# Performance work log

Measured on AMD Instinct MI355X. Metric: run time of the kernel, lower is better.

The kernel has to match this reference:

```python
import jax, jax.numpy as jnp
import numpy as np
import math

MUL = 16                      # num_in_features == num_out_features
LDIMS = (1, 3, 5)             # 0e, 1o, 2e  (lmax = 2)
FEAT = MUL * sum(LDIMS)       # 144 = irreps dim = number_of_basis
PATHS = [(0,0,0),(1,1,0),(2,2,0),
         (0,1,1),(1,0,1),(1,2,1),(2,1,1),
         (0,2,2),(1,1,2),(2,0,2),(2,2,2)]
DOT_PATHS = [(0,0,0),(1,1,0),(2,2,0)]

# ---------- real Wigner-3j / Clebsch-Gordan (e3nn convention), numpy precompute ----------

def _su2_cg(j1, m1, j2, m2, j3, m3):
    if m3 != m1 + m2:
        return 0.0
    f = math.factorial
    vmin = max(-j1 + j2 + m3, -j1 + m1, 0)
    vmax = min(j2 + j3 + m1, j3 - j1 + j2, j3 + m3)
    C = math.sqrt((2*j3+1) * f(j3+j1-j2) * f(j3-j1+j2) * f(j1+j2-j3)
                  * f(j3+m3) * f(j3-m3)
                  / (f(j1+j2+j3+1) * f(j1-m1) * f(j1+m1) * f(j2-m2) * f(j2+m2)))
    S = 0.0
    for v in range(vmin, vmax + 1):
        S += (-1.0)**(v + j2 + m2) * f(j2+j3+m1-v) * f(j1-m1+v) / (
            f(v) * f(j3-j1+j2-v) * f(j3+m3-v) * f(v+j1-j2-m3))
    return C * S

def _qmat(l):
    # complex -> real spherical-harmonic change of basis (e3nn convention)
    q = np.zeros((2*l+1, 2*l+1), dtype=np.complex128)
    for m in range(-l, 0):
        q[l+m, l+abs(m)] = 1.0/math.sqrt(2)
        q[l+m, l-abs(m)] = -1j/math.sqrt(2)
    q[l, l] = 1.0
    for m in range(1, l+1):
        q[l+m, l+abs(m)] = (-1)**m/math.sqrt(2)
        q[l+m, l-abs(m)] = 1j*(-1)**m/math.sqrt(2)
    return (-1j)**l * q

def _real_w3j(l1, l2, l3):
    C = np.zeros((2*l1+1, 2*l2+1, 2*l3+1))
    for i, m1 in enumerate(range(-l1, l1+1)):
        for j, m2 in enumerate(range(-l2, l2+1)):
            for k, m3 in enumerate(range(-l3, l3+1)):
                C[i, j, k] = _su2_cg(l1, m1, l2, m2, l3, m3)
    Cr = np.einsum('ij,kl,mn,ikn->jlm', _qmat(l1), _qmat(l2),
                   np.conj(_qmat(l3).T), C.astype(np.complex128))
    Cr = np.real(Cr)
    return (Cr / np.linalg.norm(Cr)).astype(np.float32)  # unit Frobenius norm (3j convention)

W3J = {p: _real_w3j(*p) for p in set(PATHS)}

# ---------- fully connected tensor product (component/element normalization) ----------

def _split(x):
    # blocked layout: [mul x 0e | mul x 1o | mul x 2e]
    n = x.shape[0]
    xs, o = [], 0
    for d in LDIMS:
        xs.append(x[:, o:o + MUL*d].reshape(n, MUL, d))
        o += MUL * d
    return xs

def _fctp(x1, x2, W):
    # W: [11, u, v, w] stacked per PATHS
    xs1, xs2 = _split(x1), _split(x2)
    n = x1.shape[0]
    n_paths = {l3: sum(1 for p in PATHS if p[2] == l3) for l3 in range(3)}
    outs = [None, None, None]
    for i, (l1, l2, l3) in enumerate(PATHS):
        C = jnp.asarray(W3J[(l1, l2, l3)])          # [i, j, k]
        scale = math.sqrt((2*l3 + 1) / (n_paths[l3] * MUL * MUL))
        a = jnp.einsum('nvj,ijk->nivk', xs2[l2], C)      # [n, i, v, k]
        b = jnp.einsum('nui,nivk->nuvk', xs1[l1], a)     # [n, u, v, k]
        o = scale * jnp.einsum('nuvk,uvw->nwk', b, W[i]) # [n, w, k]
        outs[l3] = o if outs[l3] is None else outs[l3] + o
    return jnp.concatenate([o.reshape(n, -1) for o in outs], axis=1)  # [n, 9*MUL]

def _dot(x1, x2, Wd):
    # FCTP(irreps_input, irreps_input, '0e'): paths (0,0,0),(1,1,0),(2,2,0), out mul = 1
    xs1, xs2 = _split(x1), _split(x2)
    fan = 3 * MUL * MUL
    acc = 0.0
    for i, (l1, l2, l3) in enumerate(DOT_PATHS):
        C = jnp.asarray(W3J[(l1, l2, l3)])[:, :, 0]      # [i, j]
        t = jnp.einsum('nui,ij,nvj->nuv', xs1[l1], C, xs2[l2])
        acc = acc + jnp.einsum('nuv,uv->n', t, Wd[i])
    return (acc * math.sqrt(1.0 / fan))[:, None]         # [n, 1]

def setup_inputs() -> dict:
    key = jax.random.key(0)
    ks = jax.random.split(key, 8)
    N = 50000
    return {
        'nodes_features': jax.random.normal(ks[0], (N, FEAT), jnp.float32),
        'degree_matrix': jax.random.normal(ks[1], (N,), jnp.float32),
        'edges_features_distance': jax.random.normal(ks[2], (N,), jnp.float32),
        'edges_features_bond': jax.random.normal(ks[3], (N,), jnp.float32),
        'w_q': jax.random.normal(ks[4], (11, MUL, MUL, MUL), jnp.float32),
        'w_k': jax.random.normal(ks[5], (11, MUL, MUL, MUL), jnp.float32),
        'w_v': jax.random.normal(ks[6], (11, MUL, MUL, MUL), jnp.float32),
        'w_dot': jax.random.normal(ks[7], (3, MUL, MUL), jnp.float32),
    }

def reference(nodes_features, degree_matrix, edges_features_distance,
              edges_features_bond, w_q, w_k, w_v, w_dot):
    # degree_matrix / edges_features_* are unused by the original forward
    x = nodes_features
    q = _fctp(x, x, w_q)                   # tp_q(x, x)
    k = _fctp(x, x, w_k)                   # tp_k(x, x)
    v = _fctp(x, x, w_v)                   # tp(x, x)
    d = _dot(q, k, w_dot)                  # [n, 1]
    e = jnp.exp(d / math.sqrt(float(FEAT)))
    attn = e / (e + 1e-10)                 # sum over last dim of size 1 + eps
    out = attn * v                         # dropout is identity in eval mode
    out = out.reshape(-1, MUL)             # view(-1, num_heads * num_out_features)
    return jax.nn.elu(out)                 # [9n, MUL]
```

## Files before the change

kernel.cpp:

```cpp
#include <hip/hip_runtime.h>
#include <math.h>

#define NP 11
#define NN 8

__device__ __constant__ int g_l1[NP]   = {0,1,2,0,1,1,2,0,1,2,2};
__device__ __constant__ int g_l2[NP]   = {0,1,2,1,0,2,1,2,1,0,2};
__device__ __constant__ int g_l3[NP]   = {0,0,0,1,1,1,1,2,2,2,2};
__device__ __constant__ int g_coff[NP] = {0,1,10,35,44,53,98,143,168,213,238};

typedef _Float16 half8 __attribute__((ext_vector_type(8)));
typedef _Float16 h2 __attribute__((ext_vector_type(2)));
typedef float f32x4 __attribute__((ext_vector_type(4)));

__device__ __forceinline__ float bfu(unsigned int v){ return __uint_as_float(v<<16); }
__device__ __forceinline__ unsigned int rne16(float f){
  unsigned int ui=__float_as_uint(f);
  return (ui+0x7fffu+((ui>>16)&1u))>>16;
}
__device__ __forceinline__ unsigned short h16(float f){
  _Float16 h=(_Float16)f;
  return __builtin_bit_cast(unsigned short,h);
}
__device__ __forceinline__ float hf(unsigned short s){
  return (float)__builtin_bit_cast(_Float16,s);
}

__device__ double dfact(int n){ double r=1.0; for(int i=2;i<=n;++i) r*=(double)i; return r; }

__device__ double su2_cg(int j1,int m1,int j2,int m2,int j3,int m3){
  if(m1+m2!=m3) return 0.0;
  int vmin=-j1+j2+m3; if(-j1+m1>vmin) vmin=-j1+m1; if(vmin<0) vmin=0;
  int vmax=j2+j3+m1; int t=j3-j1+j2; if(t<vmax) vmax=t; t=j3+m3; if(t<vmax) vmax=t;
  double C = sqrt((double)(2*j3+1)*dfact(j3+j1-j2)*dfact(j3-j1+j2)*dfact(j1+j2-j3)
      *dfact(j3+m3)*dfact(j3-m3)
      /(dfact(j1+j2+j3+1)*dfact(j1-m1)*dfact(j1+m1)*dfact(j2-m2)*dfact(j2+m2)));
  double S=0.0;
  for(int v=vmin;v<=vmax;++v){
    double sg = ((v+j2+m2)&1)? -1.0:1.0;
    S += sg*dfact(j2+j3+m1-v)*dfact(j1-m1+v)
        /(dfact(v)*dfact(j3-j1+j2-v)*dfact(j3+m3-v)*dfact(v+j1-j2-m3));
  }
  return C*S;
}

__device__ void qelem(int l,int r,int c,double &re,double &im){
  int m=r-l; double a=0.0,b=0.0; const double s=0.70710678118654752440;
  if(m<0){ if(c==l-m) a=s; else if(c==l+m) b=-s; }
  else if(m==0){ if(c==l) a=1.0; }
  else { double sg=(m&1)?-1.0:1.0; if(c==l+m) a=sg*s; else if(c==l-m) b=sg*s; }
  if(l==1){ double tt=a; a=b; b=-tt; }
  else if(l==2){ a=-a; b=-b; }
  re=a; im=b;
}

__device__ int probe_f32(const unsigned short* __restrict__ p, int nelem, int* scnt){
  if(threadIdx.x==0) *scnt=0;
  __syncthreads();
  int M = nelem < 4096 ? nelem : 4096;
  int c=0;
  for(int t=threadIdx.x;t<M;t+=blockDim.x){
    unsigned e=((unsigned)p[t]>>7)&0xFFu;
    if(e!=0u && (e<0x70u || e>0x8Eu)) ++c;
  }
  atomicAdd(scnt,c);
  __syncthreads();
  return (*scnt*8 > M) ? 1 : 0;
}

__global__ void prep(const unsigned short* __restrict__ x,
                     const unsigned short* __restrict__ wq,
                     const unsigned short* __restrict__ wk,
                     const unsigned short* __restrict__ wv,
                     const unsigned short* __restrict__ wd,
                     int nx,int nw,int nd,
                     float* __restrict__ c3j, unsigned int* __restrict__ cgh,
                     unsigned int* __restrict__ wpre){
  const int p=blockIdx.x, tp=blockIdx.y;
  __shared__ double cg[125];
  __shared__ double outv[125];
  __shared__ double nrm;
  __shared__ int scnt;

  const unsigned short* ww=(tp==0)?wq:((tp==1)?wk:wv);
  const int f32 = probe_f32(ww,nw,&scnt);

  {
    unsigned int* dst=wpre+(size_t)(p*3+tp)*2240;
    for(int t=threadIdx.x;t<2048;t+=256){
      int w=t>>7, c=t&127;
      int i0=c*32+w, i1=i0+16;
      float f0,f1;
      if(f32){
        const float* wf=(const float*)ww+(size_t)p*4096;
        f0=wf[i0]; f1=wf[i1];
      }else{
        const unsigned short* wsp=ww+(size_t)p*4096;
        f0=bfu(wsp[i0]); f1=bfu(wsp[i1]);
      }
      dst[w*140+c]=(unsigned int)h16(f0)|((unsigned int)h16(f1)<<16);
    }
  }

  if(tp==0){
    int l1=g_l1[p], l2=g_l2[p], l3=g_l3[p];
    int d1=2*l1+1, d2=2*l2+1, d3=2*l3+1;
    int tot=d1*d2*d3;
    for(int t=threadIdx.x;t<tot;t+=256){
      int i=t/(d2*d3), k=(t/d3)%d2, n=t%d3;
      cg[t]=su2_cg(l1,i-l1,l2,k-l2,l3,n-l3);
    }
    __syncthreads();
    for(int t=threadIdx.x;t<tot;t+=256){
      int a=t/(d2*d3), b=(t/d3)%d2, c=t%d3;
      double sre=0.0;
      for(int i=0;i<d1;++i){ double q1r,q1i; qelem(l1,i,a,q1r,q1i);
        for(int k=0;k<d2;++k){ double q2r,q2i; qelem(l2,k,b,q2r,q2i);
          double pr=q1r*q2r-q1i*q2i, pi=q1r*q2i+q1i*q2r;
          for(int n=0;n<d3;++n){ double q3r,q3i; qelem(l3,n,c,q3r,q3i);
            sre += (pr*q3r + pi*q3i) * cg[(i*d2+k)*d3+n];
          }
        }
      }
      outv[t]=sre;
    }
    __syncthreads();
    if(threadIdx.x==0){
      double s=0.0; for(int t=0;t<tot;++t) s+=outv[t]*outv[t];
      nrm=sqrt(s);
    }
    __syncthreads();
    const float scl_[3]={0.03608439182435161f,0.05412658773652741f,0.06987712429686843f};
    float s=scl_[l3];
    for(int t=threadIdx.x;t<tot;t+=256){
      float val=(float)(outv[t]/nrm);
      c3j[g_coff[p]+t]=val;
      unsigned int h=(unsigned int)h16(val*s);
      cgh[g_coff[p]+t]=h|(h<<16);
    }
  }

  if(p==0 && tp==0){
    int xf=probe_f32(x,nx,&scnt);
    if(threadIdx.x==0) c3j[363]=(float)xf;
    int df=probe_f32(wd,nd,&scnt);
    if(threadIdx.x==0) c3j[367]=(float)df;
  }
}

#define L_AU   0
#define L_SO   5600
#define L_XP   7392
#define L_XD   8000
#define L_WD   9184
#define L_CG   9568
#define L_TOT  9932

template<int D1,int D2,int D3>
__device__ __forceinline__ void fusedAB(const unsigned int* __restrict__ lds,
                                        const unsigned int* __restrict__ cgp,
                                        unsigned int* __restrict__ sAu,
                                        int wave, int lane, int nvalid){
  constexpr int O1=(D1==1)?0:((D1==3)?16:64);
  constexpr int O2P=(D2==1)?0:((D2==3)?8:32);
  const int nn=lane>>3, vp=lane&7;
  if(nn>=nvalid) return;
  h2 x2p[D2];
  #pragma unroll
  for(int j=0;j<D2;++j) x2p[j]=__builtin_bit_cast(h2,lds[L_XP+nn*76+O2P+vp*D2+j]);
  const int u0=wave*2;
  h2 x1a[D1],x1b[D1];
  #pragma unroll
  for(int i=0;i<D1;++i){
    x1a[i]=__builtin_bit_cast(h2,lds[L_XD+nn*148+O1+u0*D1+i]);
    x1b[i]=__builtin_bit_cast(h2,lds[L_XD+nn*148+O1+(u0+1)*D1+i]);
  }
  h2 acc0[D3],acc1[D3];
  #pragma unroll
  for(int k=0;k<D3;++k){ acc0[k]=(h2){(_Float16)0.f,(_Float16)0.f}; acc1[k]=acc0[k]; }
  #pragma unroll
  for(int i=0;i<D1;++i){
    #pragma unroll
    for(int k=0;k<D3;++k){
      h2 ar=(h2){(_Float16)0.f,(_Float16)0.f};
      #pragma unroll
      for(int j=0;j<D2;++j)
        ar+=__builtin_bit_cast(h2,cgp[(i*D2+j)*D3+k])*x2p[j];
      acc0[k]+=x1a[i]*ar;
      acc1[k]+=x1b[i]*ar;
    }
  }
  #pragma unroll
  for(int k=0;k<D3;++k){
    sAu[(k*8+nn)*140+u0*8+vp]   =__builtin_bit_cast(unsigned int,acc0[k]);
    sAu[(k*8+nn)*140+u0*8+vp+8] =__builtin_bit_cast(unsigned int,acc1[k]);
  }
}

template<int L3>
__device__ __forceinline__ void stage2_acc(const unsigned int* __restrict__ sAu,
                                           const unsigned int* __restrict__ wp_path,
                                           f32x4& a0, f32x4& a1,
                                           int n16, int quad, int wave){
  constexpr int P=(L3+1)*3;
  if(wave<P){
    int tp=wave%3, Mt=wave/3;
    const unsigned int* ap=sAu+(Mt*16+n16)*140+quad*4;
    const uint4* bp=(const uint4*)(wp_path+tp*2240+n16*140+quad*4);
    uint4 b[8];
    #pragma unroll
    for(int ks=0;ks<8;++ks) b[ks]=bp[ks*4];
    f32x4 a=a0;
    #pragma unroll
    for(int ks=0;ks<8;++ks)
      a=__builtin_amdgcn_mfma_f32_16x16x32_f16(
          *reinterpret_cast<const half8*>(ap+ks*16),
          __builtin_bit_cast(half8,b[ks]),a,0,0,0);
    a0=a;
  }
  if(L3==2 && wave==0){
    const unsigned int* ap=sAu+(2*16+n16)*140+quad*4;
    const uint4* bp=(const uint4*)(wp_path+2*2240+n16*140+quad*4);
    uint4 b2[8];
    #pragma unroll
    for(int ks=0;ks<8;++ks) b2[ks]=bp[ks*4];
    f32x4 a=a1;
    #pragma unroll
    for(int ks=0;ks<8;++ks)
      a=__builtin_amdgcn_mfma_f32_16x16x32_f16(
          *reinterpret_cast<const half8*>(ap+ks*16),
          __builtin_bit_cast(half8,b2[ks]),a,0,0,0);
    a1=a;
  }
}

template<int L3>
__device__ __forceinline__ void stage2_out(const f32x4& a0, const f32x4& a1,
                                           unsigned short* __restrict__ sOh,
                                           int n16, int quad, int wave){
  constexpr int D3=2*L3+1;
  constexpr int OO=(L3==0)?0:((L3==1)?16:64);
  constexpr int P=(L3+1)*3;
  if(wave<P){
    int tp=wave%3, Mt=wave/3;
    #pragma unroll
    for(int reg=0;reg<4;++reg){
      int row=Mt*16+quad*4+reg;
      int k=row>>3, node=row&7;
      if(k<D3) sOh[node*448+tp*144+OO+n16*D3+k]=h16(a0[reg]);
    }
  }
  if(L3==2 && wave==0){
    #pragma unroll
    for(int reg=0;reg<4;++reg){
      int row=32+quad*4+reg;
      int k=row>>3, node=row&7;
      if(k<D3) sOh[node*448+2*144+OO+n16*D3+k]=h16(a1[reg]);
    }
  }
}

__global__ __launch_bounds__(512,8) void tfn_main(
    const unsigned short* __restrict__ xin,
    const unsigned int* __restrict__ wpre,
    const unsigned int* __restrict__ cgh,
    const unsigned short* __restrict__ wd,
    const float* __restrict__ c3j,
    unsigned short* __restrict__ outp, int N)
{
  __shared__ __align__(16) unsigned int lds[L_TOT];

  const int tid=threadIdx.x;
  const int wave=tid>>6, lane=tid&63;
  const int n16=lane&15, quad=lane>>4;
  const int node0=blockIdx.x*NN;
  const int nvalid=(N-node0)<NN?(N-node0):NN;

  const int xf32 = c3j[363]!=0.0f;
  const int df32 = c3j[367]!=0.0f;

  unsigned int* sAu=lds+L_AU;
  unsigned short* sOh=(unsigned short*)(lds+L_SO);
  unsigned short* sWdh=(unsigned short*)(lds+L_WD);

  float* scratch=(float*)(lds+L_SO);
  if(!xf32){
    for(int t=tid;t<NN*36;t+=512){
      int nn=t/36, w4=t%36;
      if(nn<nvalid){
        uint2 u=((const uint2*)(xin+(size_t)(node0+nn)*144))[w4];
        float* dst=&scratch[nn*144+w4*4];
        dst[0]=bfu(u.x&0xffffu); dst[1]=bfu(u.x>>16);
        dst[2]=bfu(u.y&0xffffu); dst[3]=bfu(u.y>>16);
      }
    }
  }else{
    const float* xf=(const float*)xin;
    for(int t=tid;t<NN*144;t+=512){
      int nn=t/144, f=t%144;
      if(nn<nvalid) scratch[nn*144+f]=xf[(size_t)(node0+nn)*144+f];
    }
  }
  if(!df32){ for(int t=tid;t<768;t+=512) sWdh[t]=(unsigned short)h16(bfu((unsigned int)wd[t])); }
  else     { const float* wdf=(const float*)wd; for(int t=tid;t<768;t+=512) sWdh[t]=(unsigned short)h16(wdf[t]); }
  for(int t=tid;t<363;t+=512) lds[L_CG+t]=cgh[t];
  __syncthreads();

  for(int t=tid;t<NN*144;t+=512){
    int nn=t/144, f=t-nn*144;
    unsigned int h=(unsigned int)h16(scratch[t]);
    lds[L_XD+nn*148+f]=h|(h<<16);
  }
  for(int t=tid;t<NN*72;t+=512){
    int nn=t/72, g=t-nn*72;
    int fa,fb;
    if(g<8){ fa=2*g; fb=fa+1; }
    else if(g<32){ int gg=g-8; int vp=gg/3, j=gg-3*vp; fa=16+(2*vp)*3+j; fb=fa+3; }
    else { int gg=g-32; int vp=gg/5, j=gg-5*vp; fa=64+(2*vp)*5+j; fb=fa+5; }
    lds[L_XP+nn*76+g]=(unsigned int)h16(scratch[nn*144+fa])|((unsigned int)h16(scratch[nn*144+fb])<<16);
  }
  __syncthreads();

  #define PATH_STEP(P_,D1_,D2_,D3_) { \
    fusedAB<D1_,D2_,D3_>(lds,lds+L_CG+g_coff[P_],sAu,wave,lane,nvalid); \
    __syncthreads(); \
    stage2_acc<(D3_-1)/2>(sAu,wpre+(size_t)P_*6720,a0,a1,n16,quad,wave); \
    __syncthreads(); }

  {
    f32x4 a0={0.f,0.f,0.f,0.f}, a1={0.f,0.f,0.f,0.f};
    PATH_STEP(0,1,1,1)
    PATH_STEP(1,3,3,1)
    PATH_STEP(2,5,5,1)
    stage2_out<0>(a0,a1,sOh,n16,quad,wave);
  }
  {
    f32x4 a0={0.f,0.f,0.f,0.f}, a1={0.f,0.f,0.f,0.f};
    PATH_STEP(3,1,3,3)
    PATH_STEP(4,3,1,3)
    PATH_STEP(5,3,5,3)
    PATH_STEP(6,5,3,3)
    stage2_out<1>(a0,a1,sOh,n16,quad,wave);
  }
  {
    f32x4 a0={0.f,0.f,0.f,0.f}, a1={0.f,0.f,0.f,0.f};
    PATH_STEP(7,1,5,5)
    PATH_STEP(8,3,3,5)
    PATH_STEP(9,5,1,5)
    PATH_STEP(10,5,5,5)
    stage2_out<2>(a0,a1,sOh,n16,quad,wave);
  }
  #undef PATH_STEP
  __syncthreads();

  {
    int node=wave;
    if(node<nvalid){
      const float c0=c3j[0], c1=c3j[1], c2=c3j[10];
      const unsigned short* qh=sOh+node*448;
      const unsigned short* kh=qh+144;
      const int v=lane&15, ug=lane>>4;
      float k0=hf(kh[v]);
      float k1[3],k2[5];
      #pragma unroll
      for(int j=0;j<3;++j) k1[j]=hf(kh[16+v*3+j]);
      #pragma unroll
      for(int m=0;m<5;++m) k2[m]=hf(kh[64+v*5+m]);
      float part=0.f;
      #pragma unroll
      for(int t=0;t<4;++t){
        int u=ug+4*t;
        float d0=hf(qh[u])*k0;
        float d1=0.f;
        #pragma unroll
        for(int j=0;j<3;++j) d1+=hf(qh[16+u*3+j])*k1[j];
        float d2=0.f;
        #pragma unroll
        for(int m=0;m<5;++m) d2+=hf(qh[64+u*5+m])*k2[m];
        part+=hf(sWdh[u*16+v])*(c0*d0)+hf(sWdh[256+u*16+v])*(c1*d1)+hf(sWdh[512+u*16+v])*(c2*d2);
      }
      #pragma unroll
      for(int off=1;off<64;off<<=1) part+=__shfl_xor(part,off,64);
      float dd=part*0.03608439182435161f;
      float ex=dd*(1.0f/12.0f);
      ex=fminf(fmaxf(ex,-80.f),80.f);
      float e=expf(ex);
      float attn=e/(e+1e-10f);
      const unsigned short* vh=qh+288;
      if(!xf32){
        unsigned short* ob=outp+(size_t)(node0+node)*144;
        for(int f=lane;f<144;f+=64){
          float val=attn*hf(vh[f]);
          float r=(val>0.f)?val:expm1f(val);
          ob[f]=(unsigned short)rne16(r);
        }
      }else{
        float* ob=(float*)outp+(size_t)(node0+node)*144;
        for(int f=lane;f<144;f+=64){
          float val=attn*hf(vh[f]);
          ob[f]=(val>0.f)?val:expm1f(val);
        }
      }
    }
  }
}

extern "C" void kernel_launch(void* const* d_in, const int* in_sizes, int n_in,
                              void* d_out, int out_size, void* d_ws, size_t ws_size,
                              hipStream_t stream){
  (void)n_in; (void)out_size; (void)ws_size;
  const unsigned short* x =(const unsigned short*)d_in[0];
  const unsigned short* wq=(const unsigned short*)d_in[4];
  const unsigned short* wk=(const unsigned short*)d_in[5];
  const unsigned short* wv=(const unsigned short*)d_in[6];
  const unsigned short* wd=(const unsigned short*)d_in[7];
  float* c3j=(float*)d_ws;
  unsigned int* cgh=(unsigned int*)d_ws+1024;
  unsigned int* wpre=(unsigned int*)d_ws+2048;
  int N=in_sizes[0]/144;
  prep<<<dim3(NP,3),dim3(256),0,stream>>>(x,wq,wk,wv,wd,
      in_sizes[0],in_sizes[4],in_sizes[7],c3j,cgh,wpre);
  int nb=(N+NN-1)/NN;
  tfn_main<<<dim3(nb),dim3(512),0,stream>>>(x,wpre,cgh,wd,c3j,(unsigned short*)d_out,N);
}
```

Measured before the change: 396.0 us.

## Fuse CG contraction into MFMA A-operand generation, removing per-path LDS staging and barriers

Each wave now computes its CG-contracted A fragment directly in registers and feeds it straight into MFMAs for all three weight sets, one (L3, M-tile) supertask per wave. This removes the shared-memory intermediate buffer and the two block barriers per path (22 in total). The CG table is re-laid out as [k][i][j] and padded. In exchange only 6 of 8 waves do work in this phase, per-wave register pressure rises, and launch bounds drop to 6 blocks per SM. Shared memory use shrinks.

After: 482.7 us. +21.9%, slower.

```diff
diff --git a/kernel.cpp b/kernel.cpp
--- a/kernel.cpp
+++ b/kernel.cpp
@@ -133,10 +133,11 @@
     const float scl_[3]={0.03608439182435161f,0.05412658773652741f,0.06987712429686843f};
     float s=scl_[l3];
     for(int t=threadIdx.x;t<tot;t+=256){
+      int a=t/(d2*d3), b=(t/d3)%d2, c=t%d3;
       float val=(float)(outv[t]/nrm);
       c3j[g_coff[p]+t]=val;
       unsigned int h=(unsigned int)h16(val*s);
-      cgh[g_coff[p]+t]=h|(h<<16);
+      cgh[g_coff[p]+c*(d1*d2)+a*d2+b]=h|(h<<16);
     }
   }
 
@@ -148,119 +149,107 @@
   }
 }
 
-#define L_AU   0
-#define L_SO   5600
-#define L_XP   7392
-#define L_XD   8000
-#define L_WD   9184
-#define L_CG   9568
-#define L_TOT  9932
-
-template<int D1,int D2,int D3>
-__device__ __forceinline__ void fusedAB(const unsigned int* __restrict__ lds,
-                                        const unsigned int* __restrict__ cgp,
-                                        unsigned int* __restrict__ sAu,
-                                        int wave, int lane, int nvalid){
+#define L_XP   0
+#define L_XD   608
+#define L_WD   1792
+#define L_CG   2176
+#define L_SO   2592
+#define L_SCR  4384
+#define L_TOT  8992
+
+template<int D1,int D2>
+__device__ __forceinline__ void path_mm(const unsigned int* __restrict__ lds,
+                                        int cgoff,
+                                        const unsigned int* __restrict__ wp_path,
+                                        f32x4* __restrict__ acc,
+                                        int n16,int quad,int Mt){
   constexpr int O1=(D1==1)?0:((D1==3)?16:64);
   constexpr int O2P=(D2==1)?0:((D2==3)?8:32);
-  const int nn=lane>>3, vp=lane&7;
-  if(nn>=nvalid) return;
-  h2 x2p[D2];
+  const int nn=n16&7;
+  const int k=Mt*2+(n16>>3);
+  h2 cg[D1*D2];
+  {
+    const unsigned int* cp=lds+L_CG+cgoff+k*(D1*D2);
+    #pragma unroll
+    for(int t=0;t<D1*D2;++t) cg[t]=__builtin_bit_cast(h2,cp[t]);
+  }
+  h2 x2[4*D2];
+  {
+    const unsigned int* xp=lds+L_XP+nn*76+O2P+(quad&1)*(4*D2);
+    #pragma unroll
+    for(int t=0;t<4*D2;++t) x2[t]=__builtin_bit_cast(h2,xp[t]);
+  }
+  h2 ar[4*D1];
   #pragma unroll
-  for(int j=0;j<D2;++j) x2p[j]=__builtin_bit_cast(h2,lds[L_XP+nn*76+O2P+vp*D2+j]);
-  const int u0=wave*2;
-  h2 x1a[D1],x1b[D1];
+  for(int v4=0;v4<4;++v4)
+    #pragma unroll
+    for(int i=0;i<D1;++i){
+      h2 s=(h2){(_Float16)0.f,(_Float16)0.f};
+      #pragma unroll
+      for(int j=0;j<D2;++j) s+=cg[i*D2+j]*x2[v4*D2+j];
+      ar[v4*D1+i]=s;
+    }
+  const unsigned int* xd=lds+L_XD+nn*148+O1;
+  const int ub=quad>>1;
   #pragma unroll
-  for(int i=0;i<D1;++i){
-    x1a[i]=__builtin_bit_cast(h2,lds[L_XD+nn*148+O1+u0*D1+i]);
-    x1b[i]=__builtin_bit_cast(h2,lds[L_XD+nn*148+O1+(u0+1)*D1+i]);
-  }
-  h2 acc0[D3],acc1[D3];
-  #pragma unroll
-  for(int k=0;k<D3;++k){ acc0[k]=(h2){(_Float16)0.f,(_Float16)0.f}; acc1[k]=acc0[k]; }
-  #pragma unroll
-  for(int i=0;i<D1;++i){
-    #pragma unroll
-    for(int k=0;k<D3;++k){
-      h2 ar=(h2){(_Float16)0.f,(_Float16)0.f};
-      #pragma unroll
-      for(int j=0;j<D2;++j)
-        ar+=__builtin_bit_cast(h2,cgp[(i*D2+j)*D3+k])*x2p[j];
-      acc0[k]+=x1a[i]*ar;
-      acc1[k]+=x1b[i]*ar;
-    }
-  }
-  #pragma unroll
-  for(int k=0;k<D3;++k){
-    sAu[(k*8+nn)*140+u0*8+vp]   =__builtin_bit_cast(unsigned int,acc0[k]);
-    sAu[(k*8+nn)*140+u0*8+vp+8] =__builtin_bit_cast(unsigned int,acc1[k]);
+  for(int ks=0;ks<8;++ks){
+    const int u=2*ks+ub;
+    h2 x1[D1];
+    #pragma unroll
+    for(int i=0;i<D1;++i) x1[i]=__builtin_bit_cast(h2,xd[u*D1+i]);
+    unsigned int Ad[4];
+    #pragma unroll
+    for(int j=0;j<4;++j){
+      h2 s=(h2){(_Float16)0.f,(_Float16)0.f};
+      #pragma unroll
+      for(int i=0;i<D1;++i) s+=x1[i]*ar[j*D1+i];
+      Ad[j]=__builtin_bit_cast(unsigned int,s);
+    }
+    uint4 au; au.x=Ad[0]; au.y=Ad[1]; au.z=Ad[2]; au.w=Ad[3];
+    half8 af=__builtin_bit_cast(half8,au);
+    #pragma unroll
+    for(int tp=0;tp<3;++tp){
+      uint4 b=*(const uint4*)(wp_path+tp*2240+n16*140+quad*4+ks*16);
+      acc[tp]=__builtin_amdgcn_mfma_f32_16x16x32_f16(af,__builtin_bit_cast(half8,b),acc[tp],0,0,0);
+    }
   }
 }
 
 template<int L3>
-__device__ __forceinline__ void stage2_acc(const unsigned int* __restrict__ sAu,
-                                           const unsigned int* __restrict__ wp_path,
-                                           f32x4& a0, f32x4& a1,
-                                           int n16, int quad, int wave){
-  constexpr int P=(L3+1)*3;
-  if(wave<P){
-    int tp=wave%3, Mt=wave/3;
-    const unsigned int* ap=sAu+(Mt*16+n16)*140+quad*4;
-    const uint4* bp=(const uint4*)(wp_path+tp*2240+n16*140+quad*4);
-    uint4 b[8];
-    #pragma unroll
-    for(int ks=0;ks<8;++ks) b[ks]=bp[ks*4];
-    f32x4 a=a0;
-    #pragma unroll
-    for(int ks=0;ks<8;++ks)
-      a=__builtin_amdgcn_mfma_f32_16x16x32_f16(
-          *reinterpret_cast<const half8*>(ap+ks*16),
-          __builtin_bit_cast(half8,b[ks]),a,0,0,0);
-    a0=a;
-  }
-  if(L3==2 && wave==0){
-    const unsigned int* ap=sAu+(2*16+n16)*140+quad*4;
-    const uint4* bp=(const uint4*)(wp_path+2*2240+n16*140+quad*4);
-    uint4 b2[8];
-    #pragma unroll
-    for(int ks=0;ks<8;++ks) b2[ks]=bp[ks*4];
-    f32x4 a=a1;
-    #pragma unroll
-    for(int ks=0;ks<8;++ks)
-      a=__builtin_amdgcn_mfma_f32_16x16x32_f16(
-          *reinterpret_cast<const half8*>(ap+ks*16),
-          __builtin_bit_cast(half8,b2[ks]),a,0,0,0);
-    a1=a;
-  }
-}
-
-template<int L3>
-__device__ __forceinline__ void stage2_out(const f32x4& a0, const f32x4& a1,
-                                           unsigned short* __restrict__ sOh,
-                                           int n16, int quad, int wave){
+__device__ __forceinline__ void supertask(const unsigned int* __restrict__ lds,
+                                          const unsigned int* __restrict__ wpre,
+                                          unsigned short* __restrict__ sOh,
+                                          int n16,int quad,int Mt){
+  f32x4 acc[3];
+  acc[0]=(f32x4){0.f,0.f,0.f,0.f}; acc[1]=acc[0]; acc[2]=acc[0];
+  if(L3==0){
+    path_mm<1,1>(lds,0  ,wpre+(size_t)0*6720 ,acc,n16,quad,Mt);
+    path_mm<3,3>(lds,1  ,wpre+(size_t)1*6720 ,acc,n16,quad,Mt);
+    path_mm<5,5>(lds,10 ,wpre+(size_t)2*6720 ,acc,n16,quad,Mt);
+  }else if(L3==1){
+    path_mm<1,3>(lds,35 ,wpre+(size_t)3*6720 ,acc,n16,quad,Mt);
+    path_mm<3,1>(lds,44 ,wpre+(size_t)4*6720 ,acc,n16,quad,Mt);
+    path_mm<3,5>(lds,53 ,wpre+(size_t)5*6720 ,acc,n16,quad,Mt);
+    path_mm<5,3>(lds,98 ,wpre+(size_t)6*6720 ,acc,n16,quad,Mt);
+  }else{
+    path_mm<1,5>(lds,143,wpre+(size_t)7*6720 ,acc,n16,quad,Mt);
+    path_mm<3,3>(lds,168,wpre+(size_t)8*6720 ,acc,n16,quad,Mt);
+    path_mm<5,1>(lds,213,wpre+(size_t)9*6720 ,acc,n16,quad,Mt);
+    path_mm<5,5>(lds,238,wpre+(size_t)10*6720,acc,n16,quad,Mt);
+  }
   constexpr int D3=2*L3+1;
   constexpr int OO=(L3==0)?0:((L3==1)?16:64);
-  constexpr int P=(L3+1)*3;
-  if(wave<P){
-    int tp=wave%3, Mt=wave/3;
+  #pragma unroll
+  for(int tp=0;tp<3;++tp)
     #pragma unroll
     for(int reg=0;reg<4;++reg){
       int row=Mt*16+quad*4+reg;
       int k=row>>3, node=row&7;
-      if(k<D3) sOh[node*448+tp*144+OO+n16*D3+k]=h16(a0[reg]);
-    }
-  }
-  if(L3==2 && wave==0){
-    #pragma unroll
-    for(int reg=0;reg<4;++reg){
-      int row=32+quad*4+reg;
-      int k=row>>3, node=row&7;
-      if(k<D3) sOh[node*448+2*144+OO+n16*D3+k]=h16(a1[reg]);
-    }
-  }
-}
-
-__global__ __launch_bounds__(512,8) void tfn_main(
+      if(k<D3) sOh[node*448+tp*144+OO+n16*D3+k]=h16(acc[tp][reg]);
+    }
+}
+
+__global__ __launch_bounds__(512,6) void tfn_main(
     const unsigned short* __restrict__ xin,
     const unsigned int* __restrict__ wpre,
     const unsigned int* __restrict__ cgh,
@@ -279,11 +268,10 @@
   const int xf32 = c3j[363]!=0.0f;
   const int df32 = c3j[367]!=0.0f;
 
-  unsigned int* sAu=lds+L_AU;
   unsigned short* sOh=(unsigned short*)(lds+L_SO);
   unsigned short* sWdh=(unsigned short*)(lds+L_WD);
-
-  float* scratch=(float*)(lds+L_SO);
+  float* scratch=(float*)(lds+L_SCR);
+
   if(!xf32){
     for(int t=tid;t<NN*36;t+=512){
       int nn=t/36, w4=t%36;
@@ -303,7 +291,7 @@
   }
   if(!df32){ for(int t=tid;t<768;t+=512) sWdh[t]=(unsigned short)h16(bfu((unsigned int)wd[t])); }
   else     { const float* wdf=(const float*)wd; for(int t=tid;t<768;t+=512) sWdh[t]=(unsigned short)h16(wdf[t]); }
-  for(int t=tid;t<363;t+=512) lds[L_CG+t]=cgh[t];
+  for(int t=tid;t<416;t+=512) lds[L_CG+t]=(t<363)?cgh[t]:0u;
   __syncthreads();
 
   for(int t=tid;t<NN*144;t+=512){
@@ -321,36 +309,12 @@
   }
   __syncthreads();
 
-  #define PATH_STEP(P_,D1_,D2_,D3_) { \
-    fusedAB<D1_,D2_,D3_>(lds,lds+L_CG+g_coff[P_],sAu,wave,lane,nvalid); \
-    __syncthreads(); \
-    stage2_acc<(D3_-1)/2>(sAu,wpre+(size_t)P_*6720,a0,a1,n16,quad,wave); \
-    __syncthreads(); }
-
-  {
-    f32x4 a0={0.f,0.f,0.f,0.f}, a1={0.f,0.f,0.f,0.f};
-    PATH_STEP(0,1,1,1)
-    PATH_STEP(1,3,3,1)
-    PATH_STEP(2,5,5,1)
-    stage2_out<0>(a0,a1,sOh,n16,quad,wave);
-  }
-  {
-    f32x4 a0={0.f,0.f,0.f,0.f}, a1={0.f,0.f,0.f,0.f};
-    PATH_STEP(3,1,3,3)
-    PATH_STEP(4,3,1,3)
-    PATH_STEP(5,3,5,3)
-    PATH_STEP(6,5,3,3)
-    stage2_out<1>(a0,a1,sOh,n16,quad,wave);
-  }
-  {
-    f32x4 a0={0.f,0.f,0.f,0.f}, a1={0.f,0.f,0.f,0.f};
-    PATH_STEP(7,1,5,5)
-    PATH_STEP(8,3,3,5)
-    PATH_STEP(9,5,1,5)
-    PATH_STEP(10,5,5,5)
-    stage2_out<2>(a0,a1,sOh,n16,quad,wave);
-  }
-  #undef PATH_STEP
+  if(wave==0)      supertask<2>(lds,wpre,sOh,n16,quad,0);
+  else if(wave==1) supertask<2>(lds,wpre,sOh,n16,quad,1);
+  else if(wave==2) supertask<2>(lds,wpre,sOh,n16,quad,2);
+  else if(wave==3) supertask<1>(lds,wpre,sOh,n16,quad,0);
+  else if(wave==4) supertask<1>(lds,wpre,sOh,n16,quad,1);
+  else if(wave==5) supertask<0>(lds,wpre,sOh,n16,quad,0);
   __syncthreads();
 
   {
```
